# Kernel tuning notes

Hardware: AMD Instinct MI355X
Metric: run time of the kernel (lower is better)

## Reference

```python
import jax, jax.numpy as jnp
import numpy as np

N = 8192        # nodes
E = 49152       # edges (~avg degree 6, triangular mesh)
H = 6           # GATv2 heads
C = 512         # hidden_size (per-head out channels)
F_IN = 2 + C    # GATv2 in_channels = coord(2) + hidden(512)
ALL_FEAT = 37   # deform_in_c-2 + 16 + 16
NUM_LOOP = 3
LRELU_SLOPE = 0.2


def setup_inputs() -> dict:
    key = jax.random.key(0)
    ks = jax.random.split(key, 10)
    x = jax.random.uniform(ks[0], (N, 7), dtype=jnp.float32)
    local_feat = jax.random.normal(ks[1], (N, 16), dtype=jnp.float32)
    conv_feat = jax.random.normal(ks[2], (N, 16), dtype=jnp.float32)
    edge_index = jax.random.randint(ks[3], (2, E), 0, N, dtype=jnp.int64)
    bd_mask = jnp.zeros((N,), jnp.int32)  # poly_mesh=False path
    W_lin = jax.random.normal(ks[4], (ALL_FEAT, C), dtype=jnp.float32) / np.float32(np.sqrt(ALL_FEAT))
    b_lin = jnp.zeros((C,), jnp.float32)
    Wl = jax.random.normal(ks[5], (F_IN, H * C), dtype=jnp.float32) / np.float32(np.sqrt(F_IN))
    Wr = jax.random.normal(ks[6], (F_IN, H * C), dtype=jnp.float32) / np.float32(np.sqrt(F_IN))
    att = jax.random.normal(ks[7], (H, C), dtype=jnp.float32) / np.float32(np.sqrt(C))
    gat_bias = jnp.zeros((C,), jnp.float32)
    W_coord = jax.random.normal(ks[8], (C, 2), dtype=jnp.float32) / np.float32(np.sqrt(C))
    b_coord = jnp.zeros((2,), jnp.float32)
    return dict(x=x, local_feat=local_feat, conv_feat=conv_feat,
                W_lin=W_lin, b_lin=b_lin, Wl=Wl, Wr=Wr, att=att,
                gat_bias=gat_bias, W_coord=W_coord, b_coord=b_coord,
                edge_index=edge_index, bd_mask=bd_mask)


def _gatv2(feat, src, dst, Wl, Wr, att, bias):
    # PyG GATv2Conv: lin_l on source, lin_r on target, additive attention
    n = feat.shape[0]
    xl = (feat @ Wl).reshape(n, H, C)            # source-side transform
    xr = (feat @ Wr).reshape(n, H, C)            # target-side transform
    e = xl[src] + xr[dst]                        # [E', H, C]
    e = jax.nn.leaky_relu(e, LRELU_SLOPE)
    logits = jnp.einsum('ehc,hc->eh', e, att)    # [E', H]
    m = jax.ops.segment_max(logits, dst, num_segments=n)
    m = jnp.where(jnp.isfinite(m), m, 0.0)
    a = jnp.exp(logits - m[dst])
    denom = jax.ops.segment_sum(a, dst, num_segments=n) + 1e-16
    alpha = a / denom[dst]                       # segment softmax over incoming edges
    msg = xl[src] * alpha[:, :, None]            # [E', H, C]
    out = jax.ops.segment_sum(msg, dst, num_segments=n)  # [N, H, C]
    return out.mean(axis=1) + bias               # concat=False -> mean over heads


def reference(x, local_feat, conv_feat, W_lin, b_lin, Wl, Wr, att, gat_bias,
              W_coord, b_coord, edge_index, bd_mask):
    coord = x[:, :2]
    hidden_in = jnp.concatenate([x[:, 2:], local_feat, conv_feat], axis=1)
    hidden = jax.nn.selu(hidden_in @ W_lin + b_lin)
    # GATv2Conv adds self-loops by default
    loops = jnp.arange(N, dtype=edge_index.dtype)
    src = jnp.concatenate([edge_index[0], loops])
    dst = jnp.concatenate([edge_index[1], loops])
    for _ in range(NUM_LOOP):
        up = coord[:, 0] == 1.0
        down = coord[:, 0] == 0.0
        left = coord[:, 1] == 0.0
        right = coord[:, 1] == 1.0
        feat = jnp.concatenate([coord, hidden], axis=1)   # [N, 514]
        hidden = jax.nn.selu(_gatv2(feat, src, dst, Wl, Wr, att, gat_bias))
        out = hidden @ W_coord + b_coord                  # [N, 2]
        ox = jnp.where(down, 0.0, jnp.where(up, 1.0, out[:, 0]))
        oy = jnp.where(right, 1.0, jnp.where(left, 0.0, out[:, 1]))
        coord = jnp.stack([ox, oy], axis=1)
    return coord
```

## Files before the change

### kernel.cpp

```cpp
#include <hip/hip_runtime.h>
#include <hip/hip_bf16.h>
#include <math.h>

#define N_NODES   8192
#define NUM_E     49152
#define NUM_EDGES (NUM_E + N_NODES)
#define H_HEADS   6
#define C_DIM     512
#define HC        (H_HEADS * C_DIM)
#define XLR       (2 * HC)
#define N_FEAT    37
#define LRELU_SLOPE 0.2f
#define SELU_LAMBDA 1.0507009873554805f
#define SELU_ALPHA  1.6732632423543772f

typedef __bf16 bf16_t;
typedef bf16_t bf16x8 __attribute__((ext_vector_type(8)));
typedef float  f32x4  __attribute__((ext_vector_type(4)));
typedef float  f32x2  __attribute__((ext_vector_type(2)));

__device__ __forceinline__ int edge_src(const int* ei, int e) {
    return e < NUM_E ? ei[e] : (e - NUM_E);
}
__device__ __forceinline__ int edge_dst(const int* ei, int e) {
    return e < NUM_E ? ei[NUM_E + e] : (e - NUM_E);
}
__device__ __forceinline__ float selu_f(float v) {
    return v > 0.f ? SELU_LAMBDA * v : SELU_LAMBDA * SELU_ALPHA * (__expf(v) - 1.f);
}
__device__ __forceinline__ void gload_lds16(const void* g, void* l) {
    __builtin_amdgcn_global_load_lds((const __attribute__((address_space(1))) void*)g,
                                     (__attribute__((address_space(3))) void*)l, 16, 0, 0);
}

__global__ __launch_bounds__(512) void k_hidden0(
    const float* __restrict__ x, const float* __restrict__ lf,
    const float* __restrict__ cf, const float* __restrict__ W,
    const float* __restrict__ b, bf16_t* __restrict__ hidden,
    float* __restrict__ coord)
{
    int n = blockIdx.x;
    int c = threadIdx.x;
    __shared__ float f[N_FEAT];
    if (c < 5)            f[c] = x[n*7 + 2 + c];
    else if (c < 21)      f[c] = lf[n*16 + (c-5)];
    else if (c < N_FEAT)  f[c] = cf[n*16 + (c-21)];
    if (c < 2) coord[n*2 + c] = x[n*7 + c];
    __syncthreads();
    float acc = b[c];
    #pragma unroll
    for (int k = 0; k < N_FEAT; ++k) acc = fmaf(f[k], W[k*C_DIM + c], acc);
    hidden[n*C_DIM + c] = (bf16_t)selu_f(acc);
}

__global__ __launch_bounds__(256) void k_wt_transpose(const float* __restrict__ W,
                                                      bf16_t* __restrict__ WT)
{
    __shared__ float tile[32][33];
    int k0 = blockIdx.y * 32;
    int n0 = blockIdx.x * 32;
    int tx = threadIdx.x & 31, ty = threadIdx.x >> 5;
    #pragma unroll
    for (int i = 0; i < 4; ++i)
        tile[ty + i*8][tx] = W[(size_t)(k0 + 2 + ty + i*8) * HC + n0 + tx];
    __syncthreads();
    #pragma unroll
    for (int i = 0; i < 4; ++i)
        WT[(size_t)(n0 + ty + i*8) * C_DIM + k0 + tx] = (bf16_t)tile[tx][ty + i*8];
}

__global__ void k_hist(const int* __restrict__ ei, int* __restrict__ counts) {
    int e = blockIdx.x * blockDim.x + threadIdx.x;
    if (e >= NUM_EDGES) return;
    atomicAdd(&counts[edge_dst(ei, e)], 1);
}

__global__ __launch_bounds__(256) void k_scan(const int* __restrict__ counts,
                                              int* __restrict__ row_ptr,
                                              int* __restrict__ cursor) {
    __shared__ int part[256];
    __shared__ int off[257];
    int t = threadIdx.x;
    int base = t * 32;
    int local[32];
    int s = 0;
    #pragma unroll
    for (int i = 0; i < 32; ++i) { local[i] = s; s += counts[base + i]; }
    part[t] = s;
    __syncthreads();
    if (t == 0) {
        off[0] = 0;
        for (int i = 0; i < 256; ++i) off[i+1] = off[i] + part[i];
    }
    __syncthreads();
    int o = off[t];
    #pragma unroll
    for (int i = 0; i < 32; ++i) {
        int v = o + local[i];
        row_ptr[base + i] = v;
        cursor[base + i]  = v;
    }
    if (t == 255) row_ptr[N_NODES] = off[256];
}

__global__ void k_scatter(const int* __restrict__ ei, int* __restrict__ cursor,
                          int* __restrict__ csr_eid) {
    int e = blockIdx.x * blockDim.x + threadIdx.x;
    if (e >= NUM_EDGES) return;
    int pos = atomicAdd(&cursor[edge_dst(ei, e)], 1);
    csr_eid[pos] = e;
}

#define GM 128
#define GN 128
#define GK 32
__global__ __launch_bounds__(256) void k_gemm_bf16(
    const bf16_t* __restrict__ A,
    const bf16_t* __restrict__ BT,
    const float*  __restrict__ Wl,
    const float*  __restrict__ Wr,
    const float*  __restrict__ coord,
    bf16_t* __restrict__ out)
{
    __shared__ bf16_t As[2][GM][GK];
    __shared__ bf16_t Bs[2][GM][GK];
    int tid  = threadIdx.x;
    int wave = tid >> 6;
    int lane = tid & 63;
    int rowBase = blockIdx.y * GM;
    int colBase = blockIdx.x * GN;
    int wr = (wave >> 1) * 64;
    int wc = (wave & 1) * 64;

    f32x4 acc[4][4] = {};

    int gsw = (((lane & 3) ^ ((lane >> 3) & 3))) * 8;
    const bf16_t* Ag = A  + (size_t)(rowBase + wave*32 + (lane >> 2)) * C_DIM + gsw;
    const bf16_t* Bg = BT + (size_t)(colBase + wave*32 + (lane >> 2)) * C_DIM + gsw;
    int m16 = lane & 15;
    int q8s = (((lane >> 4) ^ ((lane >> 1) & 3))) * 8;

    gload_lds16(Ag,            &As[0][wave*32     ][0]);
    gload_lds16(Ag + 16*C_DIM, &As[0][wave*32 + 16][0]);
    gload_lds16(Bg,            &Bs[0][wave*32     ][0]);
    gload_lds16(Bg + 16*C_DIM, &Bs[0][wave*32 + 16][0]);

    int p = 0;
    for (int k0 = 0; k0 < C_DIM; k0 += GK) {
        __syncthreads();
        if (k0 + GK < C_DIM) {
            gload_lds16(Ag + k0 + GK,            &As[p^1][wave*32     ][0]);
            gload_lds16(Ag + k0 + GK + 16*C_DIM, &As[p^1][wave*32 + 16][0]);
            gload_lds16(Bg + k0 + GK,            &Bs[p^1][wave*32     ][0]);
            gload_lds16(Bg + k0 + GK + 16*C_DIM, &Bs[p^1][wave*32 + 16][0]);
        }
        bf16x8 af[4], bfr[4];
        #pragma unroll
        for (int i = 0; i < 4; ++i) af[i]  = *(const bf16x8*)&As[p][wr + i*16 + m16][q8s];
        #pragma unroll
        for (int j = 0; j < 4; ++j) bfr[j] = *(const bf16x8*)&Bs[p][wc + j*16 + m16][q8s];
        #pragma unroll
        for (int i = 0; i < 4; ++i)
            #pragma unroll
            for (int j = 0; j < 4; ++j)
                acc[i][j] = __builtin_amdgcn_mfma_f32_16x16x32_bf16(af[i], bfr[j], acc[i][j], 0, 0, 0);
        p ^= 1;
    }

    const float* Wtop = (colBase < HC) ? Wl : Wr;
    int coff = (colBase < HC) ? 0 : HC;

    int ccol  = lane & 15;
    int crow4 = (lane >> 4) * 4;
    #pragma unroll
    for (int i = 0; i < 4; ++i) {
        #pragma unroll
        for (int r = 0; r < 4; ++r) {
            int row = rowBase + wr + i*16 + crow4 + r;
            float c0 = coord[row*2 + 0], c1 = coord[row*2 + 1];
            size_t rb = (size_t)row * XLR;
            #pragma unroll
            for (int j = 0; j < 4; ++j) {
                int col = colBase + wc + j*16 + ccol;
                int wcol = col - coff;
                out[rb + col] = (bf16_t)(acc[i][j][r] + c0 * Wtop[wcol] + c1 * Wtop[HC + wcol]);
            }
        }
    }
}

#define MAX_DEG 128
__global__ __launch_bounds__(384) void k_attn_agg(
    const bf16_t* __restrict__ xlr,
    const int* __restrict__ row_ptr, const int* __restrict__ csr_eid,
    const int* __restrict__ ei, const float* __restrict__ att,
    const float* __restrict__ gat_bias, const float* __restrict__ W_coord,
    const float* __restrict__ b_coord, const float* __restrict__ coord_in,
    bf16_t* __restrict__ hidden, float* __restrict__ coord_out)
{
    int n = blockIdx.x;
    int tid = threadIdx.x;
    int h = tid >> 6, lane = tid & 63;
    __shared__ int   s_src[MAX_DEG];
    __shared__ float s_acc[HC];
    __shared__ float s_red[12];

    int beg = row_ptr[n];
    int deg = min(row_ptr[n + 1] - beg, MAX_DEG);
    for (int j = tid; j < deg; j += 384) s_src[j] = edge_src(ei, csr_eid[beg + j]);
    __syncthreads();

    size_t off = (size_t)h * C_DIM + lane * 8;
    bf16x8 xrv = *(const bf16x8*)(xlr + (size_t)n * XLR + HC + off);
    f32x2 xr2[4], at2[4], ac2[4] = {};
    #pragma unroll
    for (int i = 0; i < 4; ++i) {
        xr2[i] = f32x2{(float)xrv[2*i], (float)xrv[2*i+1]};
        at2[i] = f32x2{att[off + 2*i], att[off + 2*i + 1]};
    }

    float l = 0.f;
    int j = 0;
    for (; j + 2 <= deg; j += 2) {
        bf16x8 xa = *(const bf16x8*)(xlr + (size_t)s_src[j]     * XLR + off);
        bf16x8 xb = *(const bf16x8*)(xlr + (size_t)s_src[j + 1] * XLR + off);
        f32x2 xla[4], xlb[4];
        #pragma unroll
        for (int i = 0; i < 4; ++i) {
            xla[i] = f32x2{(float)xa[2*i], (float)xa[2*i+1]};
            xlb[i] = f32x2{(float)xb[2*i], (float)xb[2*i+1]};
        }
        f32x2 sa = {0.f, 0.f}, sb = {0.f, 0.f};
        #pragma unroll
        for (int i = 0; i < 4; ++i) {
            f32x2 va = xla[i] + xr2[i];
            f32x2 vb = xlb[i] + xr2[i];
            sa += __builtin_elementwise_max(va, va * LRELU_SLOPE) * at2[i];
            sb += __builtin_elementwise_max(vb, vb * LRELU_SLOPE) * at2[i];
        }
        float suma = sa.x + sa.y, sumb = sb.x + sb.y;
        #pragma unroll
        for (int o = 1; o < 64; o <<= 1) {
            suma += __shfl_xor(suma, o);
            sumb += __shfl_xor(sumb, o);
        }
        float aa = __expf(suma), ab = __expf(sumb);
        l += aa + ab;
        #pragma unroll
        for (int i = 0; i < 4; ++i) ac2[i] += aa * xla[i] + ab * xlb[i];
    }
    if (j < deg) {
        bf16x8 xa = *(const bf16x8*)(xlr + (size_t)s_src[j] * XLR + off);
        f32x2 xla[4];
        #pragma unroll
        for (int i = 0; i < 4; ++i) xla[i] = f32x2{(float)xa[2*i], (float)xa[2*i+1]};
        f32x2 sa = {0.f, 0.f};
        #pragma unroll
        for (int i = 0; i < 4; ++i) {
            f32x2 va = xla[i] + xr2[i];
            sa += __builtin_elementwise_max(va, va * LRELU_SLOPE) * at2[i];
        }
        float suma = sa.x + sa.y;
        #pragma unroll
        for (int o = 1; o < 64; o <<= 1) suma += __shfl_xor(suma, o);
        float aa = __expf(suma);
        l += aa;
        #pragma unroll
        for (int i = 0; i < 4; ++i) ac2[i] += aa * xla[i];
    }

    float invl = 1.f / (l + 1e-16f) * (1.f / 6.f);
    #pragma unroll
    for (int i = 0; i < 4; ++i) {
        s_acc[off + 2*i]     = ac2[i].x * invl;
        s_acc[off + 2*i + 1] = ac2[i].y * invl;
    }
    __syncthreads();

    float p0 = 0.f, p1 = 0.f;
    for (int c = tid; c < C_DIM; c += 384) {
        float s = 0.f;
        #pragma unroll
        for (int hh = 0; hh < H_HEADS; ++hh) s += s_acc[hh * C_DIM + c];
        float hv = selu_f(s + gat_bias[c]);
        hidden[n * C_DIM + c] = (bf16_t)hv;
        p0 = fmaf(hv, W_coord[c * 2 + 0], p0);
        p1 = fmaf(hv, W_coord[c * 2 + 1], p1);
    }
    #pragma unroll
    for (int o = 32; o > 0; o >>= 1) { p0 += __shfl_down(p0, o); p1 += __shfl_down(p1, o); }
    if (lane == 0) { s_red[h * 2] = p0; s_red[h * 2 + 1] = p1; }
    __syncthreads();
    if (tid == 0) {
        float o0 = b_coord[0], o1 = b_coord[1];
        #pragma unroll
        for (int w = 0; w < H_HEADS; ++w) { o0 += s_red[w * 2]; o1 += s_red[w * 2 + 1]; }
        float cx = coord_in[n * 2 + 0], cy = coord_in[n * 2 + 1];
        float ox = (cx == 0.0f) ? 0.f : ((cx == 1.0f) ? 1.f : o0);
        float oy = (cy == 1.0f) ? 1.f : ((cy == 0.0f) ? 0.f : o1);
        coord_out[n * 2 + 0] = ox;
        coord_out[n * 2 + 1] = oy;
    }
}

extern "C" void kernel_launch(void* const* d_in, const int* in_sizes, int n_in,
                              void* d_out, int out_size, void* d_ws, size_t ws_size,
                              hipStream_t stream)
{
    const float* x       = (const float*)d_in[0];
    const float* lf      = (const float*)d_in[1];
    const float* cf      = (const float*)d_in[2];
    const float* W_lin   = (const float*)d_in[3];
    const float* b_lin   = (const float*)d_in[4];
    const float* Wl      = (const float*)d_in[5];
    const float* Wr      = (const float*)d_in[6];
    const float* att     = (const float*)d_in[7];
    const float* gbias   = (const float*)d_in[8];
    const float* W_coord = (const float*)d_in[9];
    const float* b_coord = (const float*)d_in[10];
    const int*   ei      = (const int*)d_in[11];

    char* w = (char*)d_ws;
    auto alloc = [&](size_t bytes) { char* p = w; w += (bytes + 255) & ~255ull; return p; };
    bf16_t*   hidden  = (bf16_t*)alloc((size_t)N_NODES * C_DIM * 2);
    bf16_t*   WT      = (bf16_t*)alloc((size_t)XLR * C_DIM * 2);
    bf16_t*   xlr     = (bf16_t*)alloc((size_t)N_NODES * XLR * 2);
    int*      counts  = (int*)alloc((size_t)N_NODES * 4);
    int*      row_ptr = (int*)alloc((size_t)(N_NODES + 1) * 4);
    int*      cursor  = (int*)alloc((size_t)N_NODES * 4);
    int*      csr_eid = (int*)alloc((size_t)NUM_EDGES * 4);
    float*    cA      = (float*)alloc((size_t)N_NODES * 2 * 4);
    float*    cB      = (float*)alloc((size_t)N_NODES * 2 * 4);

    hipMemsetAsync(counts, 0, (size_t)N_NODES * 4, stream);
    k_hidden0<<<N_NODES, 512, 0, stream>>>(x, lf, cf, W_lin, b_lin, hidden, cA);
    {
        dim3 tg(HC / 32, C_DIM / 32);
        k_wt_transpose<<<tg, 256, 0, stream>>>(Wl, WT);
        k_wt_transpose<<<tg, 256, 0, stream>>>(Wr, WT + (size_t)HC * C_DIM);
    }
    k_hist<<<(NUM_EDGES + 255) / 256, 256, 0, stream>>>(ei, counts);
    k_scan<<<1, 256, 0, stream>>>(counts, row_ptr, cursor);
    k_scatter<<<(NUM_EDGES + 255) / 256, 256, 0, stream>>>(ei, cursor, csr_eid);

    float* cin = cA;
    for (int it = 0; it < 3; ++it) {
        float* cout = (it == 2) ? (float*)d_out : ((it == 0) ? cB : cA);
        dim3 g(XLR / GN, N_NODES / GM);
        k_gemm_bf16<<<g, 256, 0, stream>>>(hidden, WT, Wl, Wr, cin, xlr);
        k_attn_agg<<<N_NODES, 384, 0, stream>>>(xlr, row_ptr, csr_eid, ei, att,
                                                gbias, W_coord, b_coord, cin, hidden, cout);
        cin = cout;
    }
}
```

Before: 579.7 us.

## Vectorize GEMM epilogue stores, store CSR sources directly, batch nodes per attention block

The MFMA operands are swapped so each lane holds four consecutive output columns. The epilogue can then load the coordinate weights as float4 and write bf16x4 packed stores instead of scattered 2-byte stores. The CSR build now stores source node ids directly, which removes the edge-id indirection when the attention kernel loads neighbours. The attention kernel also handles 4 nodes per block in sequence to spread the att loads and launch cost, but this cuts the grid to a quarter and serializes the per-node gathers, which may reduce latency hiding.

```diff
diff --git a/kernel.cpp b/kernel.cpp
--- a/kernel.cpp
+++ b/kernel.cpp
@@ -16,6 +16,7 @@
 
 typedef __bf16 bf16_t;
 typedef bf16_t bf16x8 __attribute__((ext_vector_type(8)));
+typedef bf16_t bf16x4 __attribute__((ext_vector_type(4)));
 typedef float  f32x4  __attribute__((ext_vector_type(4)));
 typedef float  f32x2  __attribute__((ext_vector_type(2)));
 
@@ -104,11 +105,11 @@
 }
 
 __global__ void k_scatter(const int* __restrict__ ei, int* __restrict__ cursor,
-                          int* __restrict__ csr_eid) {
+                          int* __restrict__ csr_src) {
     int e = blockIdx.x * blockDim.x + threadIdx.x;
     if (e >= NUM_EDGES) return;
     int pos = atomicAdd(&cursor[edge_dst(ei, e)], 1);
-    csr_eid[pos] = e;
+    csr_src[pos] = edge_src(ei, e);
 }
 
 #define GM 128
@@ -163,143 +164,161 @@
         for (int i = 0; i < 4; ++i)
             #pragma unroll
             for (int j = 0; j < 4; ++j)
-                acc[i][j] = __builtin_amdgcn_mfma_f32_16x16x32_bf16(af[i], bfr[j], acc[i][j], 0, 0, 0);
+                acc[i][j] = __builtin_amdgcn_mfma_f32_16x16x32_bf16(bfr[j], af[i], acc[i][j], 0, 0, 0);
         p ^= 1;
     }
 
     const float* Wtop = (colBase < HC) ? Wl : Wr;
     int coff = (colBase < HC) ? 0 : HC;
-
-    int ccol  = lane & 15;
-    int crow4 = (lane >> 4) * 4;
+    int q4 = (lane >> 4) * 4;
+
+    float4 w0[4], w1[4];
+    #pragma unroll
+    for (int j = 0; j < 4; ++j) {
+        int wcol = colBase + wc + j*16 + q4 - coff;
+        w0[j] = *(const float4*)&Wtop[wcol];
+        w1[j] = *(const float4*)&Wtop[HC + wcol];
+    }
     #pragma unroll
     for (int i = 0; i < 4; ++i) {
-        #pragma unroll
-        for (int r = 0; r < 4; ++r) {
-            int row = rowBase + wr + i*16 + crow4 + r;
-            float c0 = coord[row*2 + 0], c1 = coord[row*2 + 1];
-            size_t rb = (size_t)row * XLR;
-            #pragma unroll
-            for (int j = 0; j < 4; ++j) {
-                int col = colBase + wc + j*16 + ccol;
-                int wcol = col - coff;
-                out[rb + col] = (bf16_t)(acc[i][j][r] + c0 * Wtop[wcol] + c1 * Wtop[HC + wcol]);
-            }
+        int row = rowBase + wr + i*16 + m16;
+        float c0 = coord[row*2 + 0], c1 = coord[row*2 + 1];
+        size_t rb = (size_t)row * XLR;
+        #pragma unroll
+        for (int j = 0; j < 4; ++j) {
+            int col = colBase + wc + j*16 + q4;
+            bf16x4 pk;
+            pk[0] = (bf16_t)(acc[i][j][0] + c0 * w0[j].x + c1 * w1[j].x);
+            pk[1] = (bf16_t)(acc[i][j][1] + c0 * w0[j].y + c1 * w1[j].y);
+            pk[2] = (bf16_t)(acc[i][j][2] + c0 * w0[j].z + c1 * w1[j].z);
+            pk[3] = (bf16_t)(acc[i][j][3] + c0 * w0[j].w + c1 * w1[j].w);
+            *(bf16x4*)(out + rb + col) = pk;
         }
     }
 }
 
 #define MAX_DEG 128
+#define NB 4
 __global__ __launch_bounds__(384) void k_attn_agg(
     const bf16_t* __restrict__ xlr,
-    const int* __restrict__ row_ptr, const int* __restrict__ csr_eid,
-    const int* __restrict__ ei, const float* __restrict__ att,
+    const int* __restrict__ row_ptr, const int* __restrict__ csr_src,
+    const float* __restrict__ att,
     const float* __restrict__ gat_bias, const float* __restrict__ W_coord,
     const float* __restrict__ b_coord, const float* __restrict__ coord_in,
     bf16_t* __restrict__ hidden, float* __restrict__ coord_out)
 {
-    int n = blockIdx.x;
+    int nb = blockIdx.x * NB;
     int tid = threadIdx.x;
     int h = tid >> 6, lane = tid & 63;
-    __shared__ int   s_src[MAX_DEG];
+    __shared__ int   s_src[NB][MAX_DEG];
     __shared__ float s_acc[HC];
     __shared__ float s_red[12];
 
-    int beg = row_ptr[n];
-    int deg = min(row_ptr[n + 1] - beg, MAX_DEG);
-    for (int j = tid; j < deg; j += 384) s_src[j] = edge_src(ei, csr_eid[beg + j]);
+    int degs[NB];
+    #pragma unroll
+    for (int q = 0; q < NB; ++q) {
+        int b = row_ptr[nb + q];
+        int d = min(row_ptr[nb + q + 1] - b, MAX_DEG);
+        degs[q] = d;
+        for (int j = tid; j < d; j += 384) s_src[q][j] = csr_src[b + j];
+    }
     __syncthreads();
 
     size_t off = (size_t)h * C_DIM + lane * 8;
-    bf16x8 xrv = *(const bf16x8*)(xlr + (size_t)n * XLR + HC + off);
-    f32x2 xr2[4], at2[4], ac2[4] = {};
-    #pragma unroll
-    for (int i = 0; i < 4; ++i) {
-        xr2[i] = f32x2{(float)xrv[2*i], (float)xrv[2*i+1]};
-        at2[i] = f32x2{att[off + 2*i], att[off + 2*i + 1]};
-    }
-
-    float l = 0.f;
-    int j = 0;
-    for (; j + 2 <= deg; j += 2) {
-        bf16x8 xa = *(const bf16x8*)(xlr + (size_t)s_src[j]     * XLR + off);
-        bf16x8 xb = *(const bf16x8*)(xlr + (size_t)s_src[j + 1] * XLR + off);
-        f32x2 xla[4], xlb[4];
+    f32x2 at2[4];
+    #pragma unroll
+    for (int i = 0; i < 4; ++i) at2[i] = f32x2{att[off + 2*i], att[off + 2*i + 1]};
+
+    for (int q = 0; q < NB; ++q) {
+        int n = nb + q;
+        int deg = degs[q];
+        bf16x8 xrv = *(const bf16x8*)(xlr + (size_t)n * XLR + HC + off);
+        f32x2 xr2[4], ac2[4] = {};
+        #pragma unroll
+        for (int i = 0; i < 4; ++i) xr2[i] = f32x2{(float)xrv[2*i], (float)xrv[2*i+1]};
+
+        float l = 0.f;
+        int j = 0;
+        for (; j + 2 <= deg; j += 2) {
+            bf16x8 xa = *(const bf16x8*)(xlr + (size_t)s_src[q][j]     * XLR + off);
+            bf16x8 xb = *(const bf16x8*)(xlr + (size_t)s_src[q][j + 1] * XLR + off);
+            f32x2 xla[4], xlb[4];
+            #pragma unroll
+            for (int i = 0; i < 4; ++i) {
+                xla[i] = f32x2{(float)xa[2*i], (float)xa[2*i+1]};
+                xlb[i] = f32x2{(float)xb[2*i], (float)xb[2*i+1]};
+            }
+            f32x2 sa = {0.f, 0.f}, sb = {0.f, 0.f};
+            #pragma unroll
+            for (int i = 0; i < 4; ++i) {
+                f32x2 va = xla[i] + xr2[i];
+                f32x2 vb = xlb[i] + xr2[i];
+                sa += __builtin_elementwise_max(va, va * LRELU_SLOPE) * at2[i];
+                sb += __builtin_elementwise_max(vb, vb * LRELU_SLOPE) * at2[i];
+            }
+            float suma = sa.x + sa.y, sumb = sb.x + sb.y;
+            #pragma unroll
+            for (int o = 1; o < 64; o <<= 1) {
+                suma += __shfl_xor(suma, o);
+                sumb += __shfl_xor(sumb, o);
+            }
+            float aa = __expf(suma), ab = __expf(sumb);
+            l += aa + ab;
+            #pragma unroll
+            for (int i = 0; i < 4; ++i) ac2[i] += aa * xla[i] + ab * xlb[i];
+        }
+        if (j < deg) {
+            bf16x8 xa = *(const bf16x8*)(xlr + (size_t)s_src[q][j] * XLR + off);
+            f32x2 xla[4];
+            #pragma unroll
+            for (int i = 0; i < 4; ++i) xla[i] = f32x2{(float)xa[2*i], (float)xa[2*i+1]};
+            f32x2 sa = {0.f, 0.f};
+            #pragma unroll
+            for (int i = 0; i < 4; ++i) {
+                f32x2 va = xla[i] + xr2[i];
+                sa += __builtin_elementwise_max(va, va * LRELU_SLOPE) * at2[i];
+            }
+            float suma = sa.x + sa.y;
+            #pragma unroll
+            for (int o = 1; o < 64; o <<= 1) suma += __shfl_xor(suma, o);
+            float aa = __expf(suma);
+            l += aa;
+            #pragma unroll
+            for (int i = 0; i < 4; ++i) ac2[i] += aa * xla[i];
+        }
+
+        float invl = 1.f / (l + 1e-16f) * (1.f / 6.f);
         #pragma unroll
         for (int i = 0; i < 4; ++i) {
-            xla[i] = f32x2{(float)xa[2*i], (float)xa[2*i+1]};
-            xlb[i] = f32x2{(float)xb[2*i], (float)xb[2*i+1]};
-        }
-        f32x2 sa = {0.f, 0.f}, sb = {0.f, 0.f};
-        #pragma unroll
-        for (int i = 0; i < 4; ++i) {
-            f32x2 va = xla[i] + xr2[i];
-            f32x2 vb = xlb[i] + xr2[i];
-            sa += __builtin_elementwise_max(va, va * LRELU_SLOPE) * at2[i];
-            sb += __builtin_elementwise_max(vb, vb * LRELU_SLOPE) * at2[i];
-        }
-        float suma = sa.x + sa.y, sumb = sb.x + sb.y;
-        #pragma unroll
-        for (int o = 1; o < 64; o <<= 1) {
-            suma += __shfl_xor(suma, o);
-            sumb += __shfl_xor(sumb, o);
-        }
-        float aa = __expf(suma), ab = __expf(sumb);
-        l += aa + ab;
-        #pragma unroll
-        for (int i = 0; i < 4; ++i) ac2[i] += aa * xla[i] + ab * xlb[i];
-    }
-    if (j < deg) {
-        bf16x8 xa = *(const bf16x8*)(xlr + (size_t)s_src[j] * XLR + off);
-        f32x2 xla[4];
-        #pragma unroll
-        for (int i = 0; i < 4; ++i) xla[i] = f32x2{(float)xa[2*i], (float)xa[2*i+1]};
-        f32x2 sa = {0.f, 0.f};
-        #pragma unroll
-        for (int i = 0; i < 4; ++i) {
-            f32x2 va = xla[i] + xr2[i];
-            sa += __builtin_elementwise_max(va, va * LRELU_SLOPE) * at2[i];
-        }
-        float suma = sa.x + sa.y;
-        #pragma unroll
-        for (int o = 1; o < 64; o <<= 1) suma += __shfl_xor(suma, o);
-        float aa = __expf(suma);
-        l += aa;
-        #pragma unroll
-        for (int i = 0; i < 4; ++i) ac2[i] += aa * xla[i];
-    }
-
-    float invl = 1.f / (l + 1e-16f) * (1.f / 6.f);
-    #pragma unroll
-    for (int i = 0; i < 4; ++i) {
-        s_acc[off + 2*i]     = ac2[i].x * invl;
-        s_acc[off + 2*i + 1] = ac2[i].y * invl;
-    }
-    __syncthreads();
-
-    float p0 = 0.f, p1 = 0.f;
-    for (int c = tid; c < C_DIM; c += 384) {
-        float s = 0.f;
-        #pragma unroll
-        for (int hh = 0; hh < H_HEADS; ++hh) s += s_acc[hh * C_DIM + c];
-        float hv = selu_f(s + gat_bias[c]);
-        hidden[n * C_DIM + c] = (bf16_t)hv;
-        p0 = fmaf(hv, W_coord[c * 2 + 0], p0);
-        p1 = fmaf(hv, W_coord[c * 2 + 1], p1);
-    }
-    #pragma unroll
-    for (int o = 32; o > 0; o >>= 1) { p0 += __shfl_down(p0, o); p1 += __shfl_down(p1, o); }
-    if (lane == 0) { s_red[h * 2] = p0; s_red[h * 2 + 1] = p1; }
-    __syncthreads();
-    if (tid == 0) {
-        float o0 = b_coord[0], o1 = b_coord[1];
-        #pragma unroll
-        for (int w = 0; w < H_HEADS; ++w) { o0 += s_red[w * 2]; o1 += s_red[w * 2 + 1]; }
-        float cx = coord_in[n * 2 + 0], cy = coord_in[n * 2 + 1];
-        float ox = (cx == 0.0f) ? 0.f : ((cx == 1.0f) ? 1.f : o0);
-        float oy = (cy == 1.0f) ? 1.f : ((cy == 0.0f) ? 0.f : o1);
-        coord_out[n * 2 + 0] = ox;
-        coord_out[n * 2 + 1] = oy;
+            s_acc[off + 2*i]     = ac2[i].x * invl;
+            s_acc[off + 2*i + 1] = ac2[i].y * invl;
+        }
+        __syncthreads();
+
+        float p0 = 0.f, p1 = 0.f;
+        for (int c = tid; c < C_DIM; c += 384) {
+            float s = 0.f;
+            #pragma unroll
+            for (int hh = 0; hh < H_HEADS; ++hh) s += s_acc[hh * C_DIM + c];
+            float hv = selu_f(s + gat_bias[c]);
+            hidden[n * C_DIM + c] = (bf16_t)hv;
+            p0 = fmaf(hv, W_coord[c * 2 + 0], p0);
+            p1 = fmaf(hv, W_coord[c * 2 + 1], p1);
+        }
+        #pragma unroll
+        for (int o = 32; o > 0; o >>= 1) { p0 += __shfl_down(p0, o); p1 += __shfl_down(p1, o); }
+        if (lane == 0) { s_red[h * 2] = p0; s_red[h * 2 + 1] = p1; }
+        __syncthreads();
+        if (tid == 0) {
+            float o0 = b_coord[0], o1 = b_coord[1];
+            #pragma unroll
+            for (int w = 0; w < H_HEADS; ++w) { o0 += s_red[w * 2]; o1 += s_red[w * 2 + 1]; }
+            float cx = coord_in[n * 2 + 0], cy = coord_in[n * 2 + 1];
+            float ox = (cx == 0.0f) ? 0.f : ((cx == 1.0f) ? 1.f : o0);
+            float oy = (cy == 1.0f) ? 1.f : ((cy == 0.0f) ? 0.f : o1);
+            coord_out[n * 2 + 0] = ox;
+            coord_out[n * 2 + 1] = oy;
+        }
     }
 }
 
@@ -328,7 +347,7 @@
     int*      counts  = (int*)alloc((size_t)N_NODES * 4);
     int*      row_ptr = (int*)alloc((size_t)(N_NODES + 1) * 4);
     int*      cursor  = (int*)alloc((size_t)N_NODES * 4);
-    int*      csr_eid = (int*)alloc((size_t)NUM_EDGES * 4);
+    int*      csr_src = (int*)alloc((size_t)NUM_EDGES * 4);
     float*    cA      = (float*)alloc((size_t)N_NODES * 2 * 4);
     float*    cB      = (float*)alloc((size_t)N_NODES * 2 * 4);
 
@@ -341,15 +360,15 @@
     }
     k_hist<<<(NUM_EDGES + 255) / 256, 256, 0, stream>>>(ei, counts);
     k_scan<<<1, 256, 0, stream>>>(counts, row_ptr, cursor);
-    k_scatter<<<(NUM_EDGES + 255) / 256, 256, 0, stream>>>(ei, cursor, csr_eid);
+    k_scatter<<<(NUM_EDGES + 255) / 256, 256, 0, stream>>>(ei, cursor, csr_src);
 
     float* cin = cA;
     for (int it = 0; it < 3; ++it) {
         float* cout = (it == 2) ? (float*)d_out : ((it == 0) ? cB : cA);
         dim3 g(XLR / GN, N_NODES / GM);
         k_gemm_bf16<<<g, 256, 0, stream>>>(hidden, WT, Wl, Wr, cin, xlr);
-        k_attn_agg<<<N_NODES, 384, 0, stream>>>(xlr, row_ptr, csr_eid, ei, att,
-                                                gbias, W_coord, b_coord, cin, hidden, cout);
+        k_attn_agg<<<N_NODES / NB, 384, 0, stream>>>(xlr, row_ptr, csr_src, att,
+                                                     gbias, W_coord, b_coord, cin, hidden, cout);
         cin = cout;
     }
 }
```

Result: slower. 683.9 us (+18.0%).
